# Optimization experiments

Measured on AMD Instinct MI355X. Metric: run time of the kernel, lower is better.

Reference implementation:

```python
import jax, jax.numpy as jnp
import numpy as np

B, INPUT_DIM, HIDDEN, NUM_ASSETS, NUM_HEADS = 16384, 256, 1024, 512, 4


def setup_inputs() -> dict:
    key = jax.random.key(0)
    ks = jax.random.split(key, 8)
    x = jax.random.normal(ks[0], (B, INPUT_DIM), dtype=jnp.float32)
    # last column holds the regime index as a float in {0,1,2,3}
    regime = jax.random.randint(ks[1], (B,), 0, NUM_HEADS)
    x = x.at[:, -1].set(regime.astype(jnp.float32))
    s = 0.02
    W1 = jax.random.normal(ks[2], (INPUT_DIM, HIDDEN), dtype=jnp.float32) * s
    b1 = jnp.zeros((HIDDEN,), dtype=jnp.float32)
    W2 = jax.random.normal(ks[3], (HIDDEN, HIDDEN), dtype=jnp.float32) * s
    b2 = jnp.zeros((HIDDEN,), dtype=jnp.float32)
    # 4 regime heads, stacked: [E, HIDDEN, NUM_ASSETS]
    Wh = jax.random.normal(ks[4], (NUM_HEADS, HIDDEN, NUM_ASSETS), dtype=jnp.float32) * s
    bh = jnp.zeros((NUM_HEADS, NUM_ASSETS), dtype=jnp.float32)
    return {"x": x, "W1": W1, "b1": b1, "W2": W2, "b2": b2, "Wh": Wh, "bh": bh}


def reference(x, W1, b1, W2, b2, Wh, bh):
    # regime id from last feature column (hard routing, non-differentiable)
    regime = x[:, -1].astype(jnp.int32)                      # [B]
    # dense MLP feature extractor
    h = jax.nn.relu(x @ W1 + b1)                             # [B, HIDDEN]
    h = jax.nn.relu(h @ W2 + b2)                             # [B, HIDDEN]
    # compute all 4 heads, then one-hot select (rows with regime outside
    # 0..3 get zeros, matching the torch pre-zeroed scatter semantics)
    out_all = jnp.einsum('bh,ehm->bem', h, Wh) + bh[None]    # [B, 4, NUM_ASSETS]
    onehot = (regime[:, None] == jnp.arange(NUM_HEADS)).astype(h.dtype)  # [B, 4]
    out = jnp.einsum('be,bem->bm', onehot, out_all)          # [B, NUM_ASSETS]
    alpha = jax.nn.softplus(out) + 1.0
    return alpha
```

## Files before the change

### kernel.cpp

```cpp
#include <hip/hip_runtime.h>
#include <hip/hip_bf16.h>
#include <stdint.h>

#define BSZ   16384
#define INDIM 256
#define HID   1024
#define NA    512
#define NE    4
#define BM 128
#define BN 128
#define BK 32
#define PADM (BSZ + NE * BM)

typedef __hip_bfloat16 bf16;
typedef __attribute__((ext_vector_type(8))) short    short8;
typedef __attribute__((ext_vector_type(4))) float    f32x4;
typedef __attribute__((ext_vector_type(8))) unsigned short u16x8;

__device__ __forceinline__ void gload16(const void* g, void* l) {
  __builtin_amdgcn_global_load_lds(
      (__attribute__((address_space(1))) void*)g,
      (__attribute__((address_space(3))) void*)l, 16, 0, 0);
}

__global__ void k_zero(int* cnt, int* cursor) {
  if (threadIdx.x < NE) { cnt[threadIdx.x] = 0; cursor[threadIdx.x] = 0; }
}

__global__ void k_count(const float* __restrict__ x, int* __restrict__ cnt) {
  __shared__ int h[NE];
  const int t = threadIdx.x;
  if (t < NE) h[t] = 0;
  __syncthreads();
  int i = blockIdx.x * blockDim.x + t;
  int r = (int)x[(size_t)i * INDIM + (INDIM - 1)];
  if (r >= 0 && r < NE) atomicAdd(&h[r], 1);
  __syncthreads();
  if (t < NE && h[t] > 0) atomicAdd(&cnt[t], h[t]);
}

__global__ void k_prefix(const int* __restrict__ cnt, int* __restrict__ poff) {
  if (threadIdx.x == 0) {
    int a = 0;
    for (int e = 0; e < NE; ++e) {
      poff[e] = a;
      a += (cnt[e] + BM - 1) / BM * BM;
    }
    poff[NE] = a;
  }
}

__global__ void k_scatter(const float* __restrict__ x, const int* __restrict__ poff,
                          int* __restrict__ cursor, int* __restrict__ sortidx,
                          int* __restrict__ rowid) {
  __shared__ int h[NE], base[NE];
  const int t = threadIdx.x;
  if (t < NE) h[t] = 0;
  __syncthreads();
  int i = blockIdx.x * blockDim.x + t;
  int r = (int)x[(size_t)i * INDIM + (INDIM - 1)];
  int lrank = -1;
  if (r >= 0 && r < NE) lrank = atomicAdd(&h[r], 1);
  __syncthreads();
  if (t < NE) base[t] = (h[t] > 0) ? atomicAdd(&cursor[t], h[t]) : 0;
  __syncthreads();
  if (r >= 0 && r < NE) {
    int p = poff[r] + base[r] + lrank;
    sortidx[i] = p;
    rowid[p] = i;
  }
}

__global__ void k_cast_perm(const float* __restrict__ x, const int* __restrict__ sortidx,
                            bf16* __restrict__ xb) {
  int i = blockIdx.x * blockDim.x + threadIdx.x;
  int row = i >> 5, c8 = (i & 31) * 8;
  int drow = sortidx[row];
  const float4* s = (const float4*)(x + (size_t)row * INDIM + c8);
  float4 a = s[0], b = s[1];
  bf16 t[8];
  t[0] = __float2bfloat16(a.x); t[1] = __float2bfloat16(a.y);
  t[2] = __float2bfloat16(a.z); t[3] = __float2bfloat16(a.w);
  t[4] = __float2bfloat16(b.x); t[5] = __float2bfloat16(b.y);
  t[6] = __float2bfloat16(b.z); t[7] = __float2bfloat16(b.w);
  *(u16x8*)(xb + (size_t)drow * INDIM + c8) = *(u16x8*)t;
}

__global__ void k_transpose(const float* __restrict__ src, bf16* __restrict__ dst,
                            int R, int C) {
  __shared__ float tile[32][33];
  const float* s = src + (size_t)blockIdx.z * R * C;
  bf16* d = dst + (size_t)blockIdx.z * R * C;
  int c0 = blockIdx.x * 32, r0 = blockIdx.y * 32;
  int tx = threadIdx.x, ty = threadIdx.y;
#pragma unroll
  for (int i = 0; i < 32; i += 8)
    tile[ty + i][tx] = s[(size_t)(r0 + ty + i) * C + c0 + tx];
  __syncthreads();
#pragma unroll
  for (int i = 0; i < 32; i += 8)
    d[(size_t)(c0 + ty + i) * R + r0 + tx] = __float2bfloat16(tile[tx][ty + i]);
}

__global__ __launch_bounds__(256) void k_gemm_relu(
    const bf16* __restrict__ A, const bf16* __restrict__ Bt,
    const float* __restrict__ bias, bf16* __restrict__ Out,
    int N, int K) {
  __shared__ bf16 sA[BM * BK];
  __shared__ bf16 sB[BN * BK];
  const int t = threadIdx.x, w = t >> 6, l = t & 63;
  const int wr = w >> 1, wc = w & 1;
  const int bm0 = blockIdx.y * BM, bn0 = blockIdx.x * BN;
  const int lr = l & 15, lk = (l >> 4) * 8;
  f32x4 acc[4][4] = {};

  for (int k0 = 0; k0 < K; k0 += BK) {
    __syncthreads();
#pragma unroll
    for (int s = 0; s < 2; ++s) {
      gload16(A + (size_t)(bm0 + s * 64 + (t >> 2)) * K + k0 + (t & 3) * 8,
              (char*)sA + s * 4096 + w * 1024);
      gload16(Bt + (size_t)(bn0 + s * 64 + (t >> 2)) * K + k0 + (t & 3) * 8,
              (char*)sB + s * 4096 + w * 1024);
    }
    __syncthreads();
    short8 af[4], bfr[4];
#pragma unroll
    for (int m = 0; m < 4; ++m)
      af[m] = *(const short8*)&sA[(wr * 64 + m * 16 + lr) * BK + lk];
#pragma unroll
    for (int n = 0; n < 4; ++n)
      bfr[n] = *(const short8*)&sB[(wc * 64 + n * 16 + lr) * BK + lk];
#pragma unroll
    for (int m = 0; m < 4; ++m)
#pragma unroll
      for (int n = 0; n < 4; ++n)
        acc[m][n] = __builtin_amdgcn_mfma_f32_16x16x32_bf16(af[m], bfr[n], acc[m][n], 0, 0, 0);
  }

#pragma unroll
  for (int m = 0; m < 4; ++m) {
#pragma unroll
    for (int n = 0; n < 4; ++n) {
      int col = bn0 + wc * 64 + n * 16 + lr;
      float bv = bias[col];
#pragma unroll
      for (int r = 0; r < 4; ++r) {
        int row = bm0 + wr * 64 + m * 16 + (l >> 4) * 4 + r;
        float v = acc[m][n][r] + bv;
        v = v > 0.f ? v : 0.f;
        Out[(size_t)row * N + col] = __float2bfloat16(v);
      }
    }
  }
}

__global__ __launch_bounds__(256) void k_gemm_head(
    const bf16* __restrict__ H,
    const bf16* __restrict__ Wht,
    const float* __restrict__ bh,
    const int* __restrict__ poff,
    const int* __restrict__ cnt,
    const int* __restrict__ rowid,
    float* __restrict__ Out) {
  const int mb0 = blockIdx.y * BM;
  if (mb0 >= poff[NE]) return;
  int e = 0;
#pragma unroll
  for (int k = 1; k < NE; ++k) if (mb0 >= poff[k]) e = k;
  const int pend = poff[e] + cnt[e];

  const int t = threadIdx.x, w = t >> 6, l = t & 63;
  const int wr = w >> 1, wc = w & 1;
  const int bn0 = blockIdx.x * BN;
  const int lr = l & 15, lk = (l >> 4) * 8;
  const bf16* Wt = Wht + (size_t)e * NA * HID;

  __shared__ bf16 sA[BM * BK];
  __shared__ bf16 sB[BN * BK];
  f32x4 acc[4][4] = {};

  for (int k0 = 0; k0 < HID; k0 += BK) {
    __syncthreads();
#pragma unroll
    for (int s = 0; s < 2; ++s) {
      gload16(H + (size_t)(mb0 + s * 64 + (t >> 2)) * HID + k0 + (t & 3) * 8,
              (char*)sA + s * 4096 + w * 1024);
      gload16(Wt + (size_t)(bn0 + s * 64 + (t >> 2)) * HID + k0 + (t & 3) * 8,
              (char*)sB + s * 4096 + w * 1024);
    }
    __syncthreads();
    short8 af[4], bfr[4];
#pragma unroll
    for (int m = 0; m < 4; ++m)
      af[m] = *(const short8*)&sA[(wr * 64 + m * 16 + lr) * BK + lk];
#pragma unroll
    for (int n = 0; n < 4; ++n)
      bfr[n] = *(const short8*)&sB[(wc * 64 + n * 16 + lr) * BK + lk];
#pragma unroll
    for (int m = 0; m < 4; ++m)
#pragma unroll
      for (int n = 0; n < 4; ++n)
        acc[m][n] = __builtin_amdgcn_mfma_f32_16x16x32_bf16(af[m], bfr[n], acc[m][n], 0, 0, 0);
  }

#pragma unroll
  for (int m = 0; m < 4; ++m) {
#pragma unroll
    for (int r = 0; r < 4; ++r) {
      int ps = mb0 + wr * 64 + m * 16 + (l >> 4) * 4 + r;
      if (ps < pend) {
        int row = rowid[ps];
#pragma unroll
        for (int n = 0; n < 4; ++n) {
          int col = bn0 + wc * 64 + n * 16 + lr;
          float v = acc[m][n][r] + bh[e * NA + col];
          float sp = (v > 20.f) ? v : log1pf(expf(v));
          Out[(size_t)row * NA + col] = sp + 1.f;
        }
      }
    }
  }
}

extern "C" void kernel_launch(void* const* d_in, const int* in_sizes, int n_in,
                              void* d_out, int out_size, void* d_ws, size_t ws_size,
                              hipStream_t stream) {
  const float* x  = (const float*)d_in[0];
  const float* W1 = (const float*)d_in[1];
  const float* b1 = (const float*)d_in[2];
  const float* W2 = (const float*)d_in[3];
  const float* b2 = (const float*)d_in[4];
  const float* Wh = (const float*)d_in[5];
  const float* bh = (const float*)d_in[6];
  float* out = (float*)d_out;

  char* p = (char*)d_ws;
  bf16* xb  = (bf16*)p; p += (size_t)PADM * INDIM * 2;
  bf16* w1t = (bf16*)p; p += (size_t)HID * INDIM * 2;
  bf16* w2t = (bf16*)p; p += (size_t)HID * HID * 2;
  bf16* wht = (bf16*)p; p += (size_t)NE * NA * HID * 2;
  bf16* h1b = (bf16*)p; p += (size_t)PADM * HID * 2;
  bf16* h2b = (bf16*)p; p += (size_t)PADM * HID * 2;
  int* sortidx = (int*)p; p += (size_t)BSZ * 4;
  int* rowid   = (int*)p; p += (size_t)PADM * 4;
  int* cnt    = (int*)p; p += 256;
  int* poff   = (int*)p; p += 256;
  int* cursor = (int*)p; p += 256;

  const int MB = PADM / BM;

  k_zero<<<1, 64, 0, stream>>>(cnt, cursor);
  k_count<<<BSZ / 256, 256, 0, stream>>>(x, cnt);
  k_prefix<<<1, 64, 0, stream>>>(cnt, poff);
  k_scatter<<<BSZ / 256, 256, 0, stream>>>(x, poff, cursor, sortidx, rowid);

  k_cast_perm<<<BSZ * (INDIM / 8) / 256, 256, 0, stream>>>(x, sortidx, xb);
  k_transpose<<<dim3(HID / 32, INDIM / 32, 1), dim3(32, 8), 0, stream>>>(W1, w1t, INDIM, HID);
  k_transpose<<<dim3(HID / 32, HID / 32, 1), dim3(32, 8), 0, stream>>>(W2, w2t, HID, HID);
  k_transpose<<<dim3(NA / 32, HID / 32, NE), dim3(32, 8), 0, stream>>>(Wh, wht, HID, NA);

  k_gemm_relu<<<dim3(HID / BN, MB), 256, 0, stream>>>(xb, w1t, b1, h1b, HID, INDIM);
  k_gemm_relu<<<dim3(HID / BN, MB), 256, 0, stream>>>(h1b, w2t, b2, h2b, HID, HID);
  k_gemm_head<<<dim3(NA / BN, MB), 256, 0, stream>>>(h2b, wht, bh, poff, cnt, rowid, out);
}
```

Baseline: 261.0 us.

## Double-buffer LDS tiles and swizzle workgroup order in both GEMM kernels

Both the ReLU GEMM and the routed head GEMM now use two LDS buffers. The next K-tile is prefetched with global_load_lds while MFMAs run on the current tile, which cuts one barrier per iteration and aims to hide global load latency. Workgroup IDs are also remapped with a stride-8 swizzle so neighbouring tiles land on the same XCD, for better L2 reuse. The cost is doubled LDS use, which can lower occupancy. The compiler may also insert conservative waits on the async LDS writes, which would limit the overlap.

```diff
diff --git a/kernel.cpp b/kernel.cpp
--- a/kernel.cpp
+++ b/kernel.cpp
@@ -21,6 +21,19 @@
   __builtin_amdgcn_global_load_lds(
       (__attribute__((address_space(1))) void*)g,
       (__attribute__((address_space(3))) void*)l, 16, 0, 0);
+}
+
+__device__ __forceinline__ void stage_tile(const bf16* __restrict__ A,
+                                           const bf16* __restrict__ Bt,
+                                           int bm0, int bn0, int k0, int K,
+                                           int t, int w, bf16* sa, bf16* sb) {
+#pragma unroll
+  for (int s = 0; s < 2; ++s) {
+    gload16(A + (size_t)(bm0 + s * 64 + (t >> 2)) * K + k0 + (t & 3) * 8,
+            (char*)sa + s * 4096 + w * 1024);
+    gload16(Bt + (size_t)(bn0 + s * 64 + (t >> 2)) * K + k0 + (t & 3) * 8,
+            (char*)sb + s * 4096 + w * 1024);
+  }
 }
 
 __global__ void k_zero(int* cnt, int* cursor) {
@@ -106,36 +119,37 @@
     const bf16* __restrict__ A, const bf16* __restrict__ Bt,
     const float* __restrict__ bias, bf16* __restrict__ Out,
     int N, int K) {
-  __shared__ bf16 sA[BM * BK];
-  __shared__ bf16 sB[BN * BK];
+  __shared__ bf16 sA[2][BM * BK];
+  __shared__ bf16 sB[2][BN * BK];
   const int t = threadIdx.x, w = t >> 6, l = t & 63;
   const int wr = w >> 1, wc = w & 1;
-  const int bm0 = blockIdx.y * BM, bn0 = blockIdx.x * BN;
+  const int nwg = gridDim.x * gridDim.y;
+  const int id = blockIdx.y * gridDim.x + blockIdx.x;
+  const int swz = (id & 7) * (nwg >> 3) + (id >> 3);
+  const int bm0 = (swz / gridDim.x) * BM, bn0 = (swz % gridDim.x) * BN;
   const int lr = l & 15, lk = (l >> 4) * 8;
   f32x4 acc[4][4] = {};
 
+  stage_tile(A, Bt, bm0, bn0, 0, K, t, w, sA[0], sB[0]);
+  __syncthreads();
+  int cur = 0;
   for (int k0 = 0; k0 < K; k0 += BK) {
-    __syncthreads();
-#pragma unroll
-    for (int s = 0; s < 2; ++s) {
-      gload16(A + (size_t)(bm0 + s * 64 + (t >> 2)) * K + k0 + (t & 3) * 8,
-              (char*)sA + s * 4096 + w * 1024);
-      gload16(Bt + (size_t)(bn0 + s * 64 + (t >> 2)) * K + k0 + (t & 3) * 8,
-              (char*)sB + s * 4096 + w * 1024);
-    }
-    __syncthreads();
+    const bool last = (k0 + BK >= K);
+    if (!last)
+      stage_tile(A, Bt, bm0, bn0, k0 + BK, K, t, w, sA[cur ^ 1], sB[cur ^ 1]);
     short8 af[4], bfr[4];
 #pragma unroll
     for (int m = 0; m < 4; ++m)
-      af[m] = *(const short8*)&sA[(wr * 64 + m * 16 + lr) * BK + lk];
+      af[m] = *(const short8*)&sA[cur][(wr * 64 + m * 16 + lr) * BK + lk];
 #pragma unroll
     for (int n = 0; n < 4; ++n)
-      bfr[n] = *(const short8*)&sB[(wc * 64 + n * 16 + lr) * BK + lk];
+      bfr[n] = *(const short8*)&sB[cur][(wc * 64 + n * 16 + lr) * BK + lk];
 #pragma unroll
     for (int m = 0; m < 4; ++m)
 #pragma unroll
       for (int n = 0; n < 4; ++n)
         acc[m][n] = __builtin_amdgcn_mfma_f32_16x16x32_bf16(af[m], bfr[n], acc[m][n], 0, 0, 0);
+    if (!last) { __syncthreads(); cur ^= 1; }
   }
 
 #pragma unroll
@@ -163,7 +177,11 @@
     const int* __restrict__ cnt,
     const int* __restrict__ rowid,
     float* __restrict__ Out) {
-  const int mb0 = blockIdx.y * BM;
+  const int nwg = gridDim.x * gridDim.y;
+  const int id = blockIdx.y * gridDim.x + blockIdx.x;
+  const int swz = (id & 7) * (nwg >> 3) + (id >> 3);
+  const int mb0 = (swz / gridDim.x) * BM;
+  const int bn0 = (swz % gridDim.x) * BN;
   if (mb0 >= poff[NE]) return;
   int e = 0;
 #pragma unroll
@@ -172,36 +190,33 @@
 
   const int t = threadIdx.x, w = t >> 6, l = t & 63;
   const int wr = w >> 1, wc = w & 1;
-  const int bn0 = blockIdx.x * BN;
   const int lr = l & 15, lk = (l >> 4) * 8;
   const bf16* Wt = Wht + (size_t)e * NA * HID;
 
-  __shared__ bf16 sA[BM * BK];
-  __shared__ bf16 sB[BN * BK];
+  __shared__ bf16 sA[2][BM * BK];
+  __shared__ bf16 sB[2][BN * BK];
   f32x4 acc[4][4] = {};
 
+  stage_tile(H, Wt, mb0, bn0, 0, HID, t, w, sA[0], sB[0]);
+  __syncthreads();
+  int cur = 0;
   for (int k0 = 0; k0 < HID; k0 += BK) {
-    __syncthreads();
-#pragma unroll
-    for (int s = 0; s < 2; ++s) {
-      gload16(H + (size_t)(mb0 + s * 64 + (t >> 2)) * HID + k0 + (t & 3) * 8,
-              (char*)sA + s * 4096 + w * 1024);
-      gload16(Wt + (size_t)(bn0 + s * 64 + (t >> 2)) * HID + k0 + (t & 3) * 8,
-              (char*)sB + s * 4096 + w * 1024);
-    }
-    __syncthreads();
+    const bool last = (k0 + BK >= HID);
+    if (!last)
+      stage_tile(H, Wt, mb0, bn0, k0 + BK, HID, t, w, sA[cur ^ 1], sB[cur ^ 1]);
     short8 af[4], bfr[4];
 #pragma unroll
     for (int m = 0; m < 4; ++m)
-      af[m] = *(const short8*)&sA[(wr * 64 + m * 16 + lr) * BK + lk];
+      af[m] = *(const short8*)&sA[cur][(wr * 64 + m * 16 + lr) * BK + lk];
 #pragma unroll
     for (int n = 0; n < 4; ++n)
-      bfr[n] = *(const short8*)&sB[(wc * 64 + n * 16 + lr) * BK + lk];
+      bfr[n] = *(const short8*)&sB[cur][(wc * 64 + n * 16 + lr) * BK + lk];
 #pragma unroll
     for (int m = 0; m < 4; ++m)
 #pragma unroll
       for (int n = 0; n < 4; ++n)
         acc[m][n] = __builtin_amdgcn_mfma_f32_16x16x32_bf16(af[m], bfr[n], acc[m][n], 0, 0, 0);
+    if (!last) { __syncthreads(); cur ^= 1; }
   }
 
 #pragma unroll
```

After: 291.8 us. 11.8% more time.

## Double-buffer LDS tiles in GEMM kernels to overlap global loads with MFMA

Applied to the files above, without the earlier changes.

The GEMM and head kernels now use two LDS buffers per operand and prefetch the next K-tile with global_load_lds while computing the current one. Partial vmcnt waits and raw s_barrier calls replace the two __syncthreads per iteration. The K dimension also becomes a template parameter so the loop bounds are known at compile time. The aim is to hide global memory latency behind MFMA work, at the cost of doubled LDS use, which may lower occupancy, and of hand-written waitcnt logic that depends on four loads per stage.

```diff
diff --git a/kernel.cpp b/kernel.cpp
--- a/kernel.cpp
+++ b/kernel.cpp
@@ -102,41 +102,59 @@
     d[(size_t)(c0 + ty + i) * R + r0 + tx] = __float2bfloat16(tile[tx][ty + i]);
 }
 
+#define STAGE(pa, pb, sa, sb, KK)                                       \
+  { _Pragma("unroll")                                                   \
+    for (int s = 0; s < 2; ++s) {                                       \
+      gload16((pa) + (size_t)s * 64 * (KK), (char*)(sa) + s * 4096 + w * 1024); \
+      gload16((pb) + (size_t)s * 64 * (KK), (char*)(sb) + s * 4096 + w * 1024); \
+    } }
+
+#define COMPUTE(sa, sb)                                                 \
+  { short8 af[4], bfr[4];                                               \
+    _Pragma("unroll")                                                   \
+    for (int m = 0; m < 4; ++m)                                         \
+      af[m] = *(const short8*)&(sa)[(wr * 64 + m * 16 + lr) * BK + lk]; \
+    _Pragma("unroll")                                                   \
+    for (int n = 0; n < 4; ++n)                                         \
+      bfr[n] = *(const short8*)&(sb)[(wc * 64 + n * 16 + lr) * BK + lk];\
+    _Pragma("unroll")                                                   \
+    for (int m = 0; m < 4; ++m)                                         \
+      _Pragma("unroll")                                                 \
+      for (int n = 0; n < 4; ++n)                                       \
+        acc[m][n] = __builtin_amdgcn_mfma_f32_16x16x32_bf16(af[m], bfr[n], acc[m][n], 0, 0, 0); }
+
+#define KLOOP(pa, pb, KK)                                               \
+  STAGE(pa, pb, sA[0], sB[0], KK); (pa) += BK; (pb) += BK;              \
+  _Pragma("unroll 2")                                                   \
+  for (int kt = 0; kt < (KK) / BK; ++kt) {                              \
+    if (kt + 1 < (KK) / BK) {                                           \
+      STAGE(pa, pb, sA[(kt + 1) & 1], sB[(kt + 1) & 1], KK);            \
+      (pa) += BK; (pb) += BK;                                           \
+      asm volatile("s_waitcnt vmcnt(4)" ::: "memory");                  \
+    } else {                                                            \
+      asm volatile("s_waitcnt vmcnt(0)" ::: "memory");                  \
+    }                                                                   \
+    __builtin_amdgcn_sched_barrier(0);                                  \
+    __builtin_amdgcn_s_barrier();                                       \
+    COMPUTE(sA[kt & 1], sB[kt & 1]);                                    \
+    __builtin_amdgcn_s_barrier();                                       \
+  }
+
+template <int K>
 __global__ __launch_bounds__(256) void k_gemm_relu(
     const bf16* __restrict__ A, const bf16* __restrict__ Bt,
-    const float* __restrict__ bias, bf16* __restrict__ Out,
-    int N, int K) {
-  __shared__ bf16 sA[BM * BK];
-  __shared__ bf16 sB[BN * BK];
+    const float* __restrict__ bias, bf16* __restrict__ Out, int N) {
+  __shared__ bf16 sA[2][BM * BK];
+  __shared__ bf16 sB[2][BN * BK];
   const int t = threadIdx.x, w = t >> 6, l = t & 63;
   const int wr = w >> 1, wc = w & 1;
   const int bm0 = blockIdx.y * BM, bn0 = blockIdx.x * BN;
   const int lr = l & 15, lk = (l >> 4) * 8;
   f32x4 acc[4][4] = {};
 
-  for (int k0 = 0; k0 < K; k0 += BK) {
-    __syncthreads();
-#pragma unroll
-    for (int s = 0; s < 2; ++s) {
-      gload16(A + (size_t)(bm0 + s * 64 + (t >> 2)) * K + k0 + (t & 3) * 8,
-              (char*)sA + s * 4096 + w * 1024);
-      gload16(Bt + (size_t)(bn0 + s * 64 + (t >> 2)) * K + k0 + (t & 3) * 8,
-              (char*)sB + s * 4096 + w * 1024);
-    }
-    __syncthreads();
-    short8 af[4], bfr[4];
-#pragma unroll
-    for (int m = 0; m < 4; ++m)
-      af[m] = *(const short8*)&sA[(wr * 64 + m * 16 + lr) * BK + lk];
-#pragma unroll
-    for (int n = 0; n < 4; ++n)
-      bfr[n] = *(const short8*)&sB[(wc * 64 + n * 16 + lr) * BK + lk];
-#pragma unroll
-    for (int m = 0; m < 4; ++m)
-#pragma unroll
-      for (int n = 0; n < 4; ++n)
-        acc[m][n] = __builtin_amdgcn_mfma_f32_16x16x32_bf16(af[m], bfr[n], acc[m][n], 0, 0, 0);
-  }
+  const bf16* pA = A + (size_t)(bm0 + (t >> 2)) * K + (t & 3) * 8;
+  const bf16* pB = Bt + (size_t)(bn0 + (t >> 2)) * K + (t & 3) * 8;
+  KLOOP(pA, pB, K)
 
 #pragma unroll
   for (int m = 0; m < 4; ++m) {
@@ -176,33 +194,13 @@
   const int lr = l & 15, lk = (l >> 4) * 8;
   const bf16* Wt = Wht + (size_t)e * NA * HID;
 
-  __shared__ bf16 sA[BM * BK];
-  __shared__ bf16 sB[BN * BK];
+  __shared__ bf16 sA[2][BM * BK];
+  __shared__ bf16 sB[2][BN * BK];
   f32x4 acc[4][4] = {};
 
-  for (int k0 = 0; k0 < HID; k0 += BK) {
-    __syncthreads();
-#pragma unroll
-    for (int s = 0; s < 2; ++s) {
-      gload16(H + (size_t)(mb0 + s * 64 + (t >> 2)) * HID + k0 + (t & 3) * 8,
-              (char*)sA + s * 4096 + w * 1024);
-      gload16(Wt + (size_t)(bn0 + s * 64 + (t >> 2)) * HID + k0 + (t & 3) * 8,
-              (char*)sB + s * 4096 + w * 1024);
-    }
-    __syncthreads();
-    short8 af[4], bfr[4];
-#pragma unroll
-    for (int m = 0; m < 4; ++m)
-      af[m] = *(const short8*)&sA[(wr * 64 + m * 16 + lr) * BK + lk];
-#pragma unroll
-    for (int n = 0; n < 4; ++n)
-      bfr[n] = *(const short8*)&sB[(wc * 64 + n * 16 + lr) * BK + lk];
-#pragma unroll
-    for (int m = 0; m < 4; ++m)
-#pragma unroll
-      for (int n = 0; n < 4; ++n)
-        acc[m][n] = __builtin_amdgcn_mfma_f32_16x16x32_bf16(af[m], bfr[n], acc[m][n], 0, 0, 0);
-  }
+  const bf16* pA = H + (size_t)(mb0 + (t >> 2)) * HID + (t & 3) * 8;
+  const bf16* pB = Wt + (size_t)(bn0 + (t >> 2)) * HID + (t & 3) * 8;
+  KLOOP(pA, pB, HID)
 
 #pragma unroll
   for (int m = 0; m < 4; ++m) {
@@ -260,7 +258,7 @@
   k_transpose<<<dim3(HID / 32, HID / 32, 1), dim3(32, 8), 0, stream>>>(W2, w2t, HID, HID);
   k_transpose<<<dim3(NA / 32, HID / 32, NE), dim3(32, 8), 0, stream>>>(Wh, wht, HID, NA);
 
-  k_gemm_relu<<<dim3(HID / BN, MB), 256, 0, stream>>>(xb, w1t, b1, h1b, HID, INDIM);
-  k_gemm_relu<<<dim3(HID / BN, MB), 256, 0, stream>>>(h1b, w2t, b2, h2b, HID, HID);
+  k_gemm_relu<INDIM><<<dim3(HID / BN, MB), 256, 0, stream>>>(xb, w1t, b1, h1b, HID);
+  k_gemm_relu<HID><<<dim3(HID / BN, MB), 256, 0, stream>>>(h1b, w2t, b2, h2b, HID);
   k_gemm_head<<<dim3(NA / BN, MB), 256, 0, stream>>>(h2b, wht, bh, poff, cnt, rowid, out);
 }
```

New measurement: 264.8 us. Within noise of the previous version (+1.4%).
